# Kernel tuning notes

Measured on AMD Instinct MI355X. Metric: run time of the kernel, lower is better.

## Reference

```python
import jax, jax.numpy as jnp
import numpy as np

DIM = 3072
NUM_HEADS = 24
HEAD_DIM = DIM // NUM_HEADS  # 128
EPS = 1e-6


def rms_norm(x, scale):
    # x: (..., D); torch F.rms_norm over last dim
    var = jnp.mean(jnp.square(x), axis=-1, keepdims=True)
    return x * jax.lax.rsqrt(var + EPS) * scale


def apply_rope(xq, xk, freqs_cis):
    # xq, xk: (B, H, L, D); freqs_cis: (1, 1, L, D//2, 2, 2)
    B, H, L, D = xq.shape
    xq_ = xq.astype(jnp.float32).reshape(B, H, L, D // 2, 1, 2)
    xk_ = xk.astype(jnp.float32).reshape(B, H, L, D // 2, 1, 2)
    # (1,1,L,D/2,2) * (B,H,L,D/2,1) broadcast -> (B,H,L,D/2,2)
    xq_out = freqs_cis[..., 0] * xq_[..., 0] + freqs_cis[..., 1] * xq_[..., 1]
    xk_out = freqs_cis[..., 0] * xk_[..., 0] + freqs_cis[..., 1] * xk_[..., 1]
    return xq_out.reshape(B, H, L, D).astype(xq.dtype), xk_out.reshape(B, H, L, D).astype(xk.dtype)


def setup_inputs() -> dict:
    key = jax.random.key(0)
    ks = jax.random.split(key, 7)
    B, L = 1, 2048
    x = jax.random.normal(ks[0], (B, L, DIM), dtype=jnp.float32)
    pe = jax.random.normal(ks[1], (1, 1, L, HEAD_DIM // 2, 2, 2), dtype=jnp.float32)
    # parameters (torch nn.Linear layout: weight is (out, in))
    s = 1.0 / np.sqrt(DIM)
    w_qkv = jax.random.uniform(ks[2], (3 * DIM, DIM), minval=-s, maxval=s, dtype=jnp.float32)
    w_proj = jax.random.uniform(ks[3], (DIM, DIM), minval=-s, maxval=s, dtype=jnp.float32)
    b_proj = jax.random.uniform(ks[4], (DIM,), minval=-s, maxval=s, dtype=jnp.float32)
    q_scale = jnp.ones((HEAD_DIM,), dtype=jnp.float32)
    k_scale = jnp.ones((HEAD_DIM,), dtype=jnp.float32)
    return {"x": x, "pe": pe, "w_qkv": w_qkv, "w_proj": w_proj,
            "b_proj": b_proj, "q_scale": q_scale, "k_scale": k_scale}


def reference(x, pe, w_qkv, w_proj, b_proj, q_scale, k_scale):
    B, L, _ = x.shape
    qkv = x @ w_qkv.T  # (B, L, 3*DIM)
    qkv = qkv.reshape(B, L, 3, NUM_HEADS, HEAD_DIM)
    qkv = jnp.transpose(qkv, (2, 0, 3, 1, 4))  # (3, B, H, L, D)
    q, k, v = qkv[0], qkv[1], qkv[2]
    # QKNorm (RMSNorm over head_dim)
    q = rms_norm(q, q_scale)
    k = rms_norm(k, k_scale)
    # RoPE
    q, k = apply_rope(q, k, pe)
    # SDPA: softmax(q k^T / sqrt(D)) v, non-causal
    scores = jnp.einsum("bhqd,bhkd->bhqk", q, k) / np.sqrt(HEAD_DIM).astype(np.float32)
    attn = jax.nn.softmax(scores, axis=-1)
    out = jnp.einsum("bhqk,bhkd->bhqd", attn, v)  # (B, H, L, D)
    out = jnp.transpose(out, (0, 2, 1, 3)).reshape(B, L, DIM)  # B L (H D)
    return out @ w_proj.T + b_proj
```

## Files before the change

### kernel.cpp

```cpp
#include <hip/hip_runtime.h>
#include <hip/hip_bf16.h>

typedef _Float16 f16;
typedef _Float16 f16x2 __attribute__((ext_vector_type(2)));
typedef _Float16 f16x4 __attribute__((ext_vector_type(4)));
typedef _Float16 f16x8 __attribute__((ext_vector_type(8)));
typedef float f32x4 __attribute__((ext_vector_type(4)));

#define L_SEQ 2048
#define DIM 3072
#define NHEAD 24
#define HDIM 128

__device__ __forceinline__ void gll16(const f16* g, f16* l) {
    __builtin_amdgcn_global_load_lds((const __attribute__((address_space(1))) void*)g,
                                     (__attribute__((address_space(3))) void*)l, 16, 0, 0);
}

__global__ __launch_bounds__(256) void f32_to_f16_kernel(const float* __restrict__ s,
                                                         f16* __restrict__ d, int n4) {
    int i = blockIdx.x * blockDim.x + threadIdx.x;
    int stride = gridDim.x * blockDim.x;
    for (; i < n4; i += stride) {
        float4 v = reinterpret_cast<const float4*>(s)[i];
        f16x4 o = {(f16)v.x, (f16)v.y, (f16)v.z, (f16)v.w};
        reinterpret_cast<f16x4*>(d)[i] = o;
    }
}

template <int MODE>
__global__ __launch_bounds__(256) void gemm_nt(const f16* __restrict__ A,
                                               const f16* __restrict__ B,
                                               f16* __restrict__ Cf16,
                                               float* __restrict__ Cf32,
                                               const float* __restrict__ bias,
                                               int M, int N, int K) {
    __shared__ f16 As[128 * 32];
    __shared__ f16 Bs[128 * 32];
    const int tid = threadIdx.x;
    const int wid = tid >> 6;
    const int lane = tid & 63;
    const int grp = lane >> 4;
    const int laneM = lane & 15;
    const int laneK = grp * 8;
    const int n0 = blockIdx.x * 128;
    const int m0 = blockIdx.y * 128;
    const int wr = (wid >> 1) * 64;
    const int wc = (wid & 1) * 64;

    const f32x4 vzero = {0.f, 0.f, 0.f, 0.f};
    f32x4 acc[4][4];
#pragma unroll
    for (int i = 0; i < 4; i++)
#pragma unroll
        for (int j = 0; j < 4; j++) acc[i][j] = vzero;

    const int arow = tid >> 2;
    const int acol = (tid & 3) * 8;

    for (int k0 = 0; k0 < K; k0 += 32) {
        __syncthreads();
        gll16(A + (size_t)(m0 + arow) * K + k0 + acol, &As[wid * 512]);
        gll16(A + (size_t)(m0 + 64 + arow) * K + k0 + acol, &As[2048 + wid * 512]);
        gll16(B + (size_t)(n0 + arow) * K + k0 + acol, &Bs[wid * 512]);
        gll16(B + (size_t)(n0 + 64 + arow) * K + k0 + acol, &Bs[2048 + wid * 512]);
        __syncthreads();
        f16x8 af[4], bf[4];
#pragma unroll
        for (int i = 0; i < 4; i++) {
            af[i] = *reinterpret_cast<const f16x8*>(&As[(wr + i * 16 + laneM) * 32 + laneK]);
            bf[i] = *reinterpret_cast<const f16x8*>(&Bs[(wc + i * 16 + laneM) * 32 + laneK]);
        }
#pragma unroll
        for (int i = 0; i < 4; i++)
#pragma unroll
            for (int j = 0; j < 4; j++)
                acc[i][j] = __builtin_amdgcn_mfma_f32_16x16x32_f16(af[i], bf[j], acc[i][j], 0, 0, 0);
    }

#pragma unroll
    for (int i = 0; i < 4; i++)
#pragma unroll
        for (int j = 0; j < 4; j++)
#pragma unroll
            for (int r = 0; r < 4; r++) {
                int row = m0 + wr + i * 16 + grp * 4 + r;
                int col = n0 + wc + j * 16 + laneM;
                float v = acc[i][j][r];
                if (MODE == 0) {
                    Cf16[(size_t)row * N + col] = (f16)v;
                } else {
                    Cf32[(size_t)row * N + col] = v + bias[col];
                }
            }
}

__global__ __launch_bounds__(64) void fuse_qk_kernel(const f16* __restrict__ qkv,
                                                     const float* __restrict__ pe,
                                                     const float* __restrict__ qs,
                                                     const float* __restrict__ ks,
                                                     f16* __restrict__ qb,
                                                     f16* __restrict__ kb) {
    const int l = blockIdx.x;
    const int h = blockIdx.y;
    const int i = threadIdx.x;
    const f16* row = qkv + (size_t)l * (3 * DIM) + h * HDIM;
    f16x2 qp = *reinterpret_cast<const f16x2*>(row + 2 * i);
    f16x2 kp = *reinterpret_cast<const f16x2*>(row + DIM + 2 * i);
    float q0 = (float)qp[0], q1 = (float)qp[1];
    float k0 = (float)kp[0], k1 = (float)kp[1];
    float sq = q0 * q0 + q1 * q1;
    float sk = k0 * k0 + k1 * k1;
#pragma unroll
    for (int off = 1; off < 64; off <<= 1) {
        sq += __shfl_xor(sq, off);
        sk += __shfl_xor(sk, off);
    }
    const float SCALE = 0.08838834764831845f;
    float rq = rsqrtf(sq * (1.0f / 128.0f) + 1e-6f) * SCALE;
    float rk = rsqrtf(sk * (1.0f / 128.0f) + 1e-6f);
    float4 w = *reinterpret_cast<const float4*>(pe + ((size_t)l * 64 + i) * 4);
    float qa = q0 * rq * qs[2 * i];
    float qbv = q1 * rq * qs[2 * i + 1];
    float ka = k0 * rk * ks[2 * i];
    float kbv = k1 * rk * ks[2 * i + 1];
    f16x2 qo = {(f16)(w.x * qa + w.y * qbv), (f16)(w.z * qa + w.w * qbv)};
    f16x2 ko = {(f16)(w.x * ka + w.y * kbv), (f16)(w.z * ka + w.w * kbv)};
    *reinterpret_cast<f16x2*>(qb + ((size_t)h * L_SEQ + l) * HDIM + 2 * i) = qo;
    *reinterpret_cast<f16x2*>(kb + ((size_t)h * L_SEQ + l) * HDIM + 2 * i) = ko;
}

__global__ __launch_bounds__(256) void transpose_v_kernel(const f16* __restrict__ qkv,
                                                          f16* __restrict__ vT) {
    __shared__ f16 tile[32][33];
    const int tx = threadIdx.x & 31;
    const int ty = threadIdx.x >> 5;
    const int c0 = blockIdx.x * 32;
    const int r0 = blockIdx.y * 32;
#pragma unroll
    for (int j = 0; j < 4; j++)
        tile[ty + j * 8][tx] = qkv[(size_t)(r0 + ty + j * 8) * (3 * DIM) + 2 * DIM + c0 + tx];
    __syncthreads();
#pragma unroll
    for (int j = 0; j < 4; j++)
        vT[(size_t)(c0 + ty + j * 8) * L_SEQ + r0 + tx] = tile[tx][ty + j * 8];
}

#define KVBLK 64
#define NSTEP (L_SEQ / KVBLK)

__device__ __forceinline__ void stage_kv(const f16* __restrict__ Kh,
                                         const f16* __restrict__ Vh,
                                         int k0, f16* Kt, f16* Vt, int tid) {
    const int wid = tid >> 6;
    const int krow = tid >> 4;
    const int kcl = (tid & 15) ^ (krow & 7);
    const int vrow = tid >> 3;
    const int vcl = (tid & 7) ^ (vrow & 7);
#pragma unroll
    for (int i = 0; i < 4; i++)
        gll16(Kh + (size_t)(k0 + i * 16 + krow) * HDIM + kcl * 8, Kt + i * 2048 + wid * 512);
#pragma unroll
    for (int i = 0; i < 4; i++)
        gll16(Vh + (size_t)(i * 32 + vrow) * L_SEQ + k0 + vcl * 8, Vt + i * 2048 + wid * 512);
}

__global__ __launch_bounds__(256, 2) void attn_kernel(const f16* __restrict__ qb,
                                                      const f16* __restrict__ kb,
                                                      const f16* __restrict__ vT,
                                                      f16* __restrict__ attnb) {
    __shared__ f16 Kt[2][64 * 128];
    __shared__ f16 Vt[2][128 * 64];
    __shared__ f16 Pl[4][16 * 72];
    const int tid = threadIdx.x;
    const int wid = tid >> 6;
    const int lane = tid & 63;
    const int grp = lane >> 4;
    const int laneM = lane & 15;
    const int h = blockIdx.y;
    const int q0 = blockIdx.x * 64 + wid * 16;
    const f16* Qh = qb + (size_t)h * L_SEQ * HDIM;
    const f16* Kh = kb + (size_t)h * L_SEQ * HDIM;
    const f16* Vh = vT + (size_t)h * HDIM * L_SEQ;

    f16x8 qf[4];
#pragma unroll
    for (int c = 0; c < 4; c++)
        qf[c] = *reinterpret_cast<const f16x8*>(Qh + (size_t)(q0 + laneM) * HDIM + c * 32 + grp * 8);

    const f32x4 vzero = {0.f, 0.f, 0.f, 0.f};
    f32x4 O[8];
#pragma unroll
    for (int f = 0; f < 8; f++) O[f] = vzero;
    float m = -3.0e38f;
    float lsum = 0.f;
    f16* Prow = &Pl[wid][laneM * 72];
    const int swz = laneM & 7;

    stage_kv(Kh, Vh, 0, Kt[0], Vt[0], tid);

    for (int step = 0; step < NSTEP; ++step) {
        const int cur = step & 1;
        __syncthreads();
        if (step + 1 < NSTEP)
            stage_kv(Kh, Vh, (step + 1) * KVBLK, Kt[cur ^ 1], Vt[cur ^ 1], tid);
        const f16* Kc = Kt[cur];
        const f16* Vc = Vt[cur];

        f32x4 s[4];
#pragma unroll
        for (int cc = 0; cc < 4; cc++) s[cc] = vzero;
#pragma unroll
        for (int cc = 0; cc < 4; cc++) {
            f16x8 kf[4];
#pragma unroll
            for (int c = 0; c < 4; c++)
                kf[c] = *reinterpret_cast<const f16x8*>(
                    &Kc[(cc * 16 + laneM) * 128 + (((c * 4 + grp) ^ swz) * 8)]);
#pragma unroll
            for (int c = 0; c < 4; c++)
                s[cc] = __builtin_amdgcn_mfma_f32_16x16x32_f16(kf[c], qf[c], s[cc], 0, 0, 0);
        }

        float pmax = s[0][0];
#pragma unroll
        for (int cc = 0; cc < 4; cc++)
#pragma unroll
            for (int r = 0; r < 4; r++) pmax = fmaxf(pmax, s[cc][r]);
        if (!__all(pmax <= m + 8.0f)) {
            float pm = fmaxf(pmax, __shfl_xor(pmax, 16));
            pm = fmaxf(pm, __shfl_xor(pm, 32));
            float mnew = fmaxf(m, pm);
            float alpha = __expf(m - mnew);
            m = mnew;
            lsum *= alpha;
            float af[4];
#pragma unroll
            for (int r = 0; r < 4; r++) af[r] = __shfl(alpha, grp * 4 + r);
#pragma unroll
            for (int f = 0; f < 8; f++)
#pragma unroll
                for (int r = 0; r < 4; r++) O[f][r] *= af[r];
        }
        float ps = 0.f;
#pragma unroll
        for (int cc = 0; cc < 4; cc++) {
            f16x4 pk;
#pragma unroll
            for (int r = 0; r < 4; r++) {
                float p = __expf(s[cc][r] - m);
                ps += p;
                pk[r] = (f16)p;
            }
            *reinterpret_cast<f16x4*>(Prow + cc * 16 + grp * 4) = pk;
        }
        ps += __shfl_xor(ps, 16);
        ps += __shfl_xor(ps, 32);
        lsum += ps;

#pragma unroll
        for (int z = 0; z < 2; z++) {
            f16x8 pa = *reinterpret_cast<const f16x8*>(Prow + z * 32 + grp * 8);
#pragma unroll
            for (int f = 0; f < 8; f++) {
                f16x8 vf = *reinterpret_cast<const f16x8*>(
                    &Vc[(f * 16 + laneM) * 64 + (((z * 4 + grp) ^ swz) * 8)]);
                O[f] = __builtin_amdgcn_mfma_f32_16x16x32_f16(pa, vf, O[f], 0, 0, 0);
            }
        }
    }

    float li = 1.0f / lsum;
    float lf[4];
#pragma unroll
    for (int r = 0; r < 4; r++) lf[r] = __shfl(li, grp * 4 + r);
#pragma unroll
    for (int f = 0; f < 8; f++)
#pragma unroll
        for (int r = 0; r < 4; r++) {
            int row = q0 + grp * 4 + r;
            attnb[(size_t)row * DIM + h * HDIM + f * 16 + laneM] = (f16)(O[f][r] * lf[r]);
        }
}

extern "C" void kernel_launch(void* const* d_in, const int* in_sizes, int n_in,
                              void* d_out, int out_size, void* d_ws, size_t ws_size,
                              hipStream_t stream) {
    const float* x = (const float*)d_in[0];
    const float* pe = (const float*)d_in[1];
    const float* w_qkv = (const float*)d_in[2];
    const float* w_proj = (const float*)d_in[3];
    const float* b_proj = (const float*)d_in[4];
    const float* q_scale = (const float*)d_in[5];
    const float* k_scale = (const float*)d_in[6];
    float* out = (float*)d_out;

    char* ws = (char*)d_ws;
    f16* xb     = (f16*)(ws + 0);
    f16* wqkvb  = (f16*)(ws + 12582912);
    f16* wprojb = (f16*)(ws + 69206016);
    f16* qkvb   = (f16*)(ws + 88080384);
    f16* qbuf   = (f16*)(ws + 125829120);
    f16* kbuf   = (f16*)(ws + 138412032);
    f16* vT     = (f16*)(ws + 150994944);
    f16* attnb  = (f16*)(ws + 163577856);
    if (ws_size < 176160768) return;

    f32_to_f16_kernel<<<1024, 256, 0, stream>>>(x, xb, (2048 * 3072) / 4);
    f32_to_f16_kernel<<<2048, 256, 0, stream>>>(w_qkv, wqkvb, (9216 * 3072) / 4);
    f32_to_f16_kernel<<<1024, 256, 0, stream>>>(w_proj, wprojb, (3072 * 3072) / 4);

    gemm_nt<0><<<dim3(72, 16), 256, 0, stream>>>(xb, wqkvb, qkvb, nullptr, nullptr,
                                                 2048, 9216, 3072);
    fuse_qk_kernel<<<dim3(2048, 24), 64, 0, stream>>>(qkvb, pe, q_scale, k_scale, qbuf, kbuf);
    transpose_v_kernel<<<dim3(96, 64), 256, 0, stream>>>(qkvb, vT);
    attn_kernel<<<dim3(32, 24), 256, 0, stream>>>(qbuf, kbuf, vT, attnb);
    gemm_nt<1><<<dim3(24, 16), 256, 0, stream>>>(attnb, wprojb, nullptr, out, b_proj,
                                                 2048, 3072, 3072);
}
```

Before: 417.3 us.

## Rewrite GEMMs with 4-stage LDS pipeline, 256x128 tiles and swizzled LDS

Replaces the single-buffered 128x128 GEMM with a 512-thread kernel using 256x128 tiles and a 4-slot LDS ring. Global-to-LDS loads are issued three k-steps ahead, and the code waits with explicit vmcnt counts and one barrier per step instead of two. An XOR swizzle on the LDS column avoids bank conflicts, and s_setprio raises priority during the MFMA block. This is meant to hide global load latency and cut sync overhead, at the cost of more LDS per block (96KB) and fewer blocks for the projection GEMM.

Measured after the change: 397.5 us. 4.7% less time.

```diff
diff --git a/kernel.cpp b/kernel.cpp
--- a/kernel.cpp
+++ b/kernel.cpp
@@ -28,25 +28,63 @@
     }
 }
 
+
+#define GEMM_BODY(T, VM, DO_STAGE)                                                      \
+    {                                                                                   \
+        asm volatile("s_waitcnt vmcnt(" #VM ")" ::: "memory");                          \
+        __builtin_amdgcn_s_barrier();                                                   \
+        __builtin_amdgcn_sched_barrier(0);                                              \
+        const int slot_ = (T) & 3;                                                      \
+        f16x8 af[4], bf[4];                                                             \
+        _Pragma("unroll") for (int i = 0; i < 4; i++)                                   \
+            af[i] = *reinterpret_cast<const f16x8*>(                                    \
+                &As[slot_][(wr + i * 16 + laneM) * 32 + fc16]);                         \
+        _Pragma("unroll") for (int j = 0; j < 4; j++)                                   \
+            bf[j] = *reinterpret_cast<const f16x8*>(                                    \
+                &Bs[slot_][(wc + j * 16 + laneM) * 32 + fc16]);                         \
+        if (DO_STAGE) {                                                                 \
+            const int t3 = (T) + 3;                                                     \
+            const int s3 = t3 & 3;                                                      \
+            gll16(Asrc0 + t3 * 32, &As[s3][dstoff]);                                    \
+            gll16(Asrc1 + t3 * 32, &As[s3][4096 + dstoff]);                             \
+            gll16(Bsrc + t3 * 32, &Bs[s3][dstoff]);                                     \
+        }                                                                               \
+        __builtin_amdgcn_s_setprio(1);                                                  \
+        _Pragma("unroll") for (int i = 0; i < 4; i++)                                   \
+            _Pragma("unroll") for (int j = 0; j < 4; j++)                               \
+                acc[i][j] =                                                             \
+                    __builtin_amdgcn_mfma_f32_16x16x32_f16(af[i], bf[j], acc[i][j],     \
+                                                           0, 0, 0);                    \
+        __builtin_amdgcn_s_setprio(0);                                                  \
+    }
+
 template <int MODE>
-__global__ __launch_bounds__(256) void gemm_nt(const f16* __restrict__ A,
+__global__ __launch_bounds__(512) void rg_gemm(const f16* __restrict__ A,
                                                const f16* __restrict__ B,
                                                f16* __restrict__ Cf16,
                                                float* __restrict__ Cf32,
                                                const float* __restrict__ bias,
                                                int M, int N, int K) {
-    __shared__ f16 As[128 * 32];
-    __shared__ f16 Bs[128 * 32];
+    __shared__ f16 As[4][256 * 32];
+    __shared__ f16 Bs[4][128 * 32];
     const int tid = threadIdx.x;
     const int wid = tid >> 6;
     const int lane = tid & 63;
     const int grp = lane >> 4;
     const int laneM = lane & 15;
-    const int laneK = grp * 8;
+    const int m0 = blockIdx.y * 256;
     const int n0 = blockIdx.x * 128;
-    const int m0 = blockIdx.y * 128;
     const int wr = (wid >> 1) * 64;
     const int wc = (wid & 1) * 64;
+    const int NT = K >> 5;
+    const int fc16 = (grp ^ ((laneM >> 1) & 3)) * 8;
+
+    const int srow = tid >> 2;
+    const int scol = (((tid & 3) ^ ((tid >> 3) & 3)) << 3);
+    const f16* Asrc0 = A + (size_t)(m0 + srow) * K + scol;
+    const f16* Asrc1 = A + (size_t)(m0 + 128 + srow) * K + scol;
+    const f16* Bsrc = B + (size_t)(n0 + srow) * K + scol;
+    const int dstoff = wid * 512;
 
     const f32x4 vzero = {0.f, 0.f, 0.f, 0.f};
     f32x4 acc[4][4];
@@ -55,28 +93,19 @@
 #pragma unroll
         for (int j = 0; j < 4; j++) acc[i][j] = vzero;
 
-    const int arow = tid >> 2;
-    const int acol = (tid & 3) * 8;
-
-    for (int k0 = 0; k0 < K; k0 += 32) {
-        __syncthreads();
-        gll16(A + (size_t)(m0 + arow) * K + k0 + acol, &As[wid * 512]);
-        gll16(A + (size_t)(m0 + 64 + arow) * K + k0 + acol, &As[2048 + wid * 512]);
-        gll16(B + (size_t)(n0 + arow) * K + k0 + acol, &Bs[wid * 512]);
-        gll16(B + (size_t)(n0 + 64 + arow) * K + k0 + acol, &Bs[2048 + wid * 512]);
-        __syncthreads();
-        f16x8 af[4], bf[4];
-#pragma unroll
-        for (int i = 0; i < 4; i++) {
-            af[i] = *reinterpret_cast<const f16x8*>(&As[(wr + i * 16 + laneM) * 32 + laneK]);
-            bf[i] = *reinterpret_cast<const f16x8*>(&Bs[(wc + i * 16 + laneM) * 32 + laneK]);
-        }
-#pragma unroll
-        for (int i = 0; i < 4; i++)
-#pragma unroll
-            for (int j = 0; j < 4; j++)
-                acc[i][j] = __builtin_amdgcn_mfma_f32_16x16x32_f16(af[i], bf[j], acc[i][j], 0, 0, 0);
-    }
+#pragma unroll
+    for (int t = 0; t < 3; t++) {
+        const int s = t & 3;
+        gll16(Asrc0 + t * 32, &As[s][dstoff]);
+        gll16(Asrc1 + t * 32, &As[s][4096 + dstoff]);
+        gll16(Bsrc + t * 32, &Bs[s][dstoff]);
+    }
+
+    int t = 0;
+    for (; t < NT - 3; ++t) GEMM_BODY(t, 6, true);
+    GEMM_BODY(t, 6, false); ++t;
+    GEMM_BODY(t, 3, false); ++t;
+    GEMM_BODY(t, 0, false);
 
 #pragma unroll
     for (int i = 0; i < 4; i++)
@@ -310,11 +339,11 @@
     f32_to_f16_kernel<<<2048, 256, 0, stream>>>(w_qkv, wqkvb, (9216 * 3072) / 4);
     f32_to_f16_kernel<<<1024, 256, 0, stream>>>(w_proj, wprojb, (3072 * 3072) / 4);
 
-    gemm_nt<0><<<dim3(72, 16), 256, 0, stream>>>(xb, wqkvb, qkvb, nullptr, nullptr,
-                                                 2048, 9216, 3072);
+    rg_gemm<0><<<dim3(72, 8), 512, 0, stream>>>(xb, wqkvb, qkvb, nullptr, nullptr,
+                                                2048, 9216, 3072);
     fuse_qk_kernel<<<dim3(2048, 24), 64, 0, stream>>>(qkvb, pe, q_scale, k_scale, qbuf, kbuf);
     transpose_v_kernel<<<dim3(96, 64), 256, 0, stream>>>(qkvb, vT);
     attn_kernel<<<dim3(32, 24), 256, 0, stream>>>(qbuf, kbuf, vT, attnb);
-    gemm_nt<1><<<dim3(24, 16), 256, 0, stream>>>(attnb, wprojb, nullptr, out, b_proj,
-                                                 2048, 3072, 3072);
-}
+    rg_gemm<1><<<dim3(24, 8), 512, 0, stream>>>(attnb, wprojb, nullptr, out, b_proj,
+                                                2048, 3072, 3072);
+}
```

## Replace GEMMs with double-buffered 256x256 pipelined kernel and fuse V transpose

Applied to the files above, without the earlier changes.

Replaces the simple single-buffered 128x128 GEMM with a 512-thread, 256x256-tile kernel. It double-buffers LDS with async global-to-LDS loads interleaved between MFMA phases, uses explicit waitcnt, barriers and priority hints, swizzles the LDS layout and remaps workgroups. The QKV GEMM epilogue now writes V directly in transposed layout, which removes the separate transpose kernel. The QK norm kernel now packs 4 heads per block. The larger tiles mean fewer blocks (288 and 96), so CU occupancy on the output projection is low, and the hand-tuned sync schedule is fragile.

New measurement: 486.9 us. +16.7%, slower.

```diff
diff --git a/kernel.cpp b/kernel.cpp
--- a/kernel.cpp
+++ b/kernel.cpp
@@ -28,82 +28,191 @@
     }
 }
 
+
+#define PH8_MFMA(RH)                                                                    \
+    __builtin_amdgcn_s_setprio(1);                                                      \
+    _Pragma("unroll") for (int fr = 0; fr < 4; fr++)                                    \
+        _Pragma("unroll") for (int fc = 0; fc < 4; fc++)                                \
+            acc[RH][fr][fc] = __builtin_amdgcn_mfma_f32_16x16x32_f16(                   \
+                af[fr], bf[fc], acc[RH][fr][fc], 0, 0, 0);                              \
+    __builtin_amdgcn_s_setprio(0);
+
+#define PH8_BODY(T, VMA, VMB, DO_STAGE)                                                 \
+    {                                                                                   \
+        const int s_ = (T) & 1;                                                         \
+        const f16* Asl = &As[s_][0];                                                    \
+        const f16* Bsl = &Bs[s_][0];                                                    \
+        f16* Ao = &As[s_ ^ 1][0];                                                       \
+        f16* Bo = &Bs[s_ ^ 1][0];                                                       \
+        const int tn = ((T) + 1) * 64;                                                  \
+        f16x8 af[4], bf[4];                                                             \
+                                                     \
+        asm volatile("s_waitcnt vmcnt(" #VMA ")" ::: "memory");                         \
+        __builtin_amdgcn_s_barrier();                                                   \
+        __builtin_amdgcn_sched_barrier(0);                                              \
+        _Pragma("unroll") for (int fc = 0; fc < 4; fc++)                                \
+            bf[fc] = *reinterpret_cast<const f16x8*>(                                   \
+                &Bsl[(wc + fc * 16 + laneM) * 32 + fcg]);                               \
+        _Pragma("unroll") for (int fr = 0; fr < 4; fr++)                                \
+            af[fr] = *reinterpret_cast<const f16x8*>(                                   \
+                &Asl[(wr + fr * 16 + laneM) * 32 + fcg]);                               \
+        if (DO_STAGE) { gll16(sA0 + tn, Ao + dst); gll16(sA1 + tn, Ao + 4096 + dst); }  \
+        __builtin_amdgcn_sched_barrier(0);                                              \
+        __builtin_amdgcn_s_barrier();                                                   \
+        PH8_MFMA(0)                                                                     \
+                                         \
+        __builtin_amdgcn_s_barrier();                                                   \
+        __builtin_amdgcn_sched_barrier(0);                                              \
+        _Pragma("unroll") for (int fr = 0; fr < 4; fr++)                                \
+            af[fr] = *reinterpret_cast<const f16x8*>(                                   \
+                &Asl[(wr + 64 + fr * 16 + laneM) * 32 + fcg]);                          \
+        if (DO_STAGE) { gll16(sB0 + tn, Bo + dst); gll16(sB1 + tn, Bo + 4096 + dst); }  \
+        __builtin_amdgcn_sched_barrier(0);                                              \
+        __builtin_amdgcn_s_barrier();                                                   \
+        PH8_MFMA(1)                                                                     \
+                                                     \
+        asm volatile("s_waitcnt vmcnt(" #VMB ")" ::: "memory");                         \
+        __builtin_amdgcn_s_barrier();                                                   \
+        __builtin_amdgcn_sched_barrier(0);                                              \
+        _Pragma("unroll") for (int fc = 0; fc < 4; fc++)                                \
+            bf[fc] = *reinterpret_cast<const f16x8*>(                                   \
+                &Bsl[8192 + (wc + fc * 16 + laneM) * 32 + fcg]);                        \
+        _Pragma("unroll") for (int fr = 0; fr < 4; fr++)                                \
+            af[fr] = *reinterpret_cast<const f16x8*>(                                   \
+                &Asl[8192 + (wr + fr * 16 + laneM) * 32 + fcg]);                        \
+        if (DO_STAGE) {                                                                 \
+            gll16(sA0 + tn + 32, Ao + 8192 + dst);                                      \
+            gll16(sA1 + tn + 32, Ao + 8192 + 4096 + dst);                               \
+        }                                                                               \
+        __builtin_amdgcn_sched_barrier(0);                                              \
+        __builtin_amdgcn_s_barrier();                                                   \
+        PH8_MFMA(0)                                                                     \
+                                         \
+        __builtin_amdgcn_s_barrier();                                                   \
+        __builtin_amdgcn_sched_barrier(0);                                              \
+        _Pragma("unroll") for (int fr = 0; fr < 4; fr++)                                \
+            af[fr] = *reinterpret_cast<const f16x8*>(                                   \
+                &Asl[8192 + (wr + 64 + fr * 16 + laneM) * 32 + fcg]);                   \
+        if (DO_STAGE) {                                                                 \
+            gll16(sB0 + tn + 32, Bo + 8192 + dst);                                      \
+            gll16(sB1 + tn + 32, Bo + 8192 + 4096 + dst);                               \
+        }                                                                               \
+        __builtin_amdgcn_sched_barrier(0);                                              \
+        __builtin_amdgcn_s_barrier();                                                   \
+        PH8_MFMA(1)                                                                     \
+    }
+
 template <int MODE>
-__global__ __launch_bounds__(256) void gemm_nt(const f16* __restrict__ A,
-                                               const f16* __restrict__ B,
-                                               f16* __restrict__ Cf16,
-                                               float* __restrict__ Cf32,
-                                               const float* __restrict__ bias,
-                                               int M, int N, int K) {
-    __shared__ f16 As[128 * 32];
-    __shared__ f16 Bs[128 * 32];
+__global__ __launch_bounds__(512, 2) void ph8_gemm(const f16* __restrict__ A,
+                                                   const f16* __restrict__ B,
+                                                   f16* __restrict__ Cf16,
+                                                   f16* __restrict__ vT,
+                                                   float* __restrict__ Cf32,
+                                                   const float* __restrict__ bias,
+                                                   int M, int N, int K) {
+    __shared__ f16 As[2][2 * 256 * 32];
+    __shared__ f16 Bs[2][2 * 256 * 32];
     const int tid = threadIdx.x;
     const int wid = tid >> 6;
     const int lane = tid & 63;
     const int grp = lane >> 4;
     const int laneM = lane & 15;
-    const int laneK = grp * 8;
-    const int n0 = blockIdx.x * 128;
-    const int m0 = blockIdx.y * 128;
-    const int wr = (wid >> 1) * 64;
-    const int wc = (wid & 1) * 64;
+
+    const int nwg = gridDim.x * gridDim.y;
+    const int orig = blockIdx.y * gridDim.x + blockIdx.x;
+    const int wgid = (orig & 7) * (nwg >> 3) + (orig >> 3);
+    const int by = wgid % gridDim.y;
+    const int bx = wgid / gridDim.y;
+    const int m0 = by * 256;
+    const int n0 = bx * 256;
+
+    const int wr = (wid >> 2) * 128;
+    const int wc = (wid & 3) * 64;
+    const int NT = K >> 6;
+    const int fcg = (grp ^ ((laneM >> 1) & 3)) * 8;
+
+    const int sglog = ((tid & 3) ^ ((tid >> 3) & 3)) * 8;
+    const int srow = tid >> 2;
+    const f16* sA0 = A + (size_t)(m0 + srow) * K + sglog;
+    const f16* sA1 = A + (size_t)(m0 + 128 + srow) * K + sglog;
+    const f16* sB0 = B + (size_t)(n0 + srow) * K + sglog;
+    const f16* sB1 = B + (size_t)(n0 + 128 + srow) * K + sglog;
+    const int dst = wid * 512;
 
     const f32x4 vzero = {0.f, 0.f, 0.f, 0.f};
-    f32x4 acc[4][4];
-#pragma unroll
-    for (int i = 0; i < 4; i++)
-#pragma unroll
-        for (int j = 0; j < 4; j++) acc[i][j] = vzero;
-
-    const int arow = tid >> 2;
-    const int acol = (tid & 3) * 8;
-
-    for (int k0 = 0; k0 < K; k0 += 32) {
-        __syncthreads();
-        gll16(A + (size_t)(m0 + arow) * K + k0 + acol, &As[wid * 512]);
-        gll16(A + (size_t)(m0 + 64 + arow) * K + k0 + acol, &As[2048 + wid * 512]);
-        gll16(B + (size_t)(n0 + arow) * K + k0 + acol, &Bs[wid * 512]);
-        gll16(B + (size_t)(n0 + 64 + arow) * K + k0 + acol, &Bs[2048 + wid * 512]);
-        __syncthreads();
-        f16x8 af[4], bf[4];
-#pragma unroll
-        for (int i = 0; i < 4; i++) {
-            af[i] = *reinterpret_cast<const f16x8*>(&As[(wr + i * 16 + laneM) * 32 + laneK]);
-            bf[i] = *reinterpret_cast<const f16x8*>(&Bs[(wc + i * 16 + laneM) * 32 + laneK]);
-        }
+    f32x4 acc[2][4][4];
+#pragma unroll
+    for (int h = 0; h < 2; h++)
 #pragma unroll
         for (int i = 0; i < 4; i++)
 #pragma unroll
-            for (int j = 0; j < 4; j++)
-                acc[i][j] = __builtin_amdgcn_mfma_f32_16x16x32_f16(af[i], bf[j], acc[i][j], 0, 0, 0);
+            for (int j = 0; j < 4; j++) acc[h][i][j] = vzero;
+
+    gll16(sA0, &As[0][dst]);
+    gll16(sA1, &As[0][4096 + dst]);
+    gll16(sB0, &Bs[0][dst]);
+    gll16(sB1, &Bs[0][4096 + dst]);
+    gll16(sA0 + 32, &As[0][8192 + dst]);
+    gll16(sA1 + 32, &As[0][8192 + 4096 + dst]);
+    gll16(sB0 + 32, &Bs[0][8192 + dst]);
+    gll16(sB1 + 32, &Bs[0][8192 + 4096 + dst]);
+
+    int t = 0;
+    for (; t < NT - 1; ++t) PH8_BODY(t, 4, 4, true);
+    PH8_BODY(t, 4, 0, false);
+
+    if (MODE == 1) {
+#pragma unroll
+        for (int h = 0; h < 2; h++)
+#pragma unroll
+            for (int fr = 0; fr < 4; fr++)
+#pragma unroll
+                for (int fc = 0; fc < 4; fc++)
+#pragma unroll
+                    for (int r = 0; r < 4; r++) {
+                        int row = m0 + wr + h * 64 + fr * 16 + grp * 4 + r;
+                        int col = n0 + wc + fc * 16 + laneM;
+                        Cf32[(size_t)row * N + col] = acc[h][fr][fc][r] + bias[col];
+                    }
+    } else if (n0 < 2 * DIM) {
+#pragma unroll
+        for (int h = 0; h < 2; h++)
+#pragma unroll
+            for (int fr = 0; fr < 4; fr++)
+#pragma unroll
+                for (int fc = 0; fc < 4; fc++)
+#pragma unroll
+                    for (int r = 0; r < 4; r++) {
+                        int row = m0 + wr + h * 64 + fr * 16 + grp * 4 + r;
+                        int col = n0 + wc + fc * 16 + laneM;
+                        Cf16[(size_t)row * N + col] = (f16)acc[h][fr][fc][r];
+                    }
+    } else {
+#pragma unroll
+        for (int h = 0; h < 2; h++)
+#pragma unroll
+            for (int fr = 0; fr < 4; fr++)
+#pragma unroll
+                for (int fc = 0; fc < 4; fc++) {
+                    int hd = n0 - 2 * DIM + wc + fc * 16 + laneM;
+                    int row0 = m0 + wr + h * 64 + fr * 16 + grp * 4;
+                    f16x4 pk;
+#pragma unroll
+                    for (int r = 0; r < 4; r++) pk[r] = (f16)acc[h][fr][fc][r];
+                    *reinterpret_cast<f16x4*>(&vT[(size_t)hd * L_SEQ + row0]) = pk;
+                }
     }
-
-#pragma unroll
-    for (int i = 0; i < 4; i++)
-#pragma unroll
-        for (int j = 0; j < 4; j++)
-#pragma unroll
-            for (int r = 0; r < 4; r++) {
-                int row = m0 + wr + i * 16 + grp * 4 + r;
-                int col = n0 + wc + j * 16 + laneM;
-                float v = acc[i][j][r];
-                if (MODE == 0) {
-                    Cf16[(size_t)row * N + col] = (f16)v;
-                } else {
-                    Cf32[(size_t)row * N + col] = v + bias[col];
-                }
-            }
-}
-
-__global__ __launch_bounds__(64) void fuse_qk_kernel(const f16* __restrict__ qkv,
-                                                     const float* __restrict__ pe,
-                                                     const float* __restrict__ qs,
-                                                     const float* __restrict__ ks,
-                                                     f16* __restrict__ qb,
-                                                     f16* __restrict__ kb) {
+}
+
+__global__ __launch_bounds__(256) void fuse_qk_kernel(const f16* __restrict__ qkv,
+                                                      const float* __restrict__ pe,
+                                                      const float* __restrict__ qs,
+                                                      const float* __restrict__ ks,
+                                                      f16* __restrict__ qb,
+                                                      f16* __restrict__ kb) {
     const int l = blockIdx.x;
-    const int h = blockIdx.y;
-    const int i = threadIdx.x;
+    const int h = blockIdx.y * 4 + (threadIdx.x >> 6);
+    const int i = threadIdx.x & 63;
     const f16* row = qkv + (size_t)l * (3 * DIM) + h * HDIM;
     f16x2 qp = *reinterpret_cast<const f16x2*>(row + 2 * i);
     f16x2 kp = *reinterpret_cast<const f16x2*>(row + DIM + 2 * i);
@@ -128,22 +237,6 @@
     f16x2 ko = {(f16)(w.x * ka + w.y * kbv), (f16)(w.z * ka + w.w * kbv)};
     *reinterpret_cast<f16x2*>(qb + ((size_t)h * L_SEQ + l) * HDIM + 2 * i) = qo;
     *reinterpret_cast<f16x2*>(kb + ((size_t)h * L_SEQ + l) * HDIM + 2 * i) = ko;
-}
-
-__global__ __launch_bounds__(256) void transpose_v_kernel(const f16* __restrict__ qkv,
-                                                          f16* __restrict__ vT) {
-    __shared__ f16 tile[32][33];
-    const int tx = threadIdx.x & 31;
-    const int ty = threadIdx.x >> 5;
-    const int c0 = blockIdx.x * 32;
-    const int r0 = blockIdx.y * 32;
-#pragma unroll
-    for (int j = 0; j < 4; j++)
-        tile[ty + j * 8][tx] = qkv[(size_t)(r0 + ty + j * 8) * (3 * DIM) + 2 * DIM + c0 + tx];
-    __syncthreads();
-#pragma unroll
-    for (int j = 0; j < 4; j++)
-        vT[(size_t)(c0 + ty + j * 8) * L_SEQ + r0 + tx] = tile[tx][ty + j * 8];
 }
 
 #define KVBLK 64
@@ -310,11 +403,10 @@
     f32_to_f16_kernel<<<2048, 256, 0, stream>>>(w_qkv, wqkvb, (9216 * 3072) / 4);
     f32_to_f16_kernel<<<1024, 256, 0, stream>>>(w_proj, wprojb, (3072 * 3072) / 4);
 
-    gemm_nt<0><<<dim3(72, 16), 256, 0, stream>>>(xb, wqkvb, qkvb, nullptr, nullptr,
+    ph8_gemm<0><<<dim3(36, 8), 512, 0, stream>>>(xb, wqkvb, qkvb, vT, nullptr, nullptr,
                                                  2048, 9216, 3072);
-    fuse_qk_kernel<<<dim3(2048, 24), 64, 0, stream>>>(qkvb, pe, q_scale, k_scale, qbuf, kbuf);
-    transpose_v_kernel<<<dim3(96, 64), 256, 0, stream>>>(qkvb, vT);
+    fuse_qk_kernel<<<dim3(2048, 6), 256, 0, stream>>>(qkvb, pe, q_scale, k_scale, qbuf, kbuf);
     attn_kernel<<<dim3(32, 24), 256, 0, stream>>>(qbuf, kbuf, vT, attnb);
-    gemm_nt<1><<<dim3(24, 16), 256, 0, stream>>>(attnb, wprojb, nullptr, out, b_proj,
+    ph8_gemm<1><<<dim3(12, 8), 512, 0, stream>>>(attnb, wprojb, nullptr, nullptr, out, b_proj,
                                                  2048, 3072, 3072);
 }
```
